# Optimization experiments

Measured on AMD Instinct MI355X. Metric: run time of the kernel, lower is better.

The kernel has to match this reference:

```python
import jax, jax.numpy as jnp
import numpy as np
from jax.ops import segment_sum, segment_min, segment_max

N, E = 25000, 400000
NF, EF = 30, 10
H = 40          # n_hidden (multiple of towers)
T = 5           # towers
F = H           # F_in per tower (divide_input=False)
FO = H // T     # F_out per tower
L = 2           # gnn layers
NC = 2          # classes
EPS_BN = 1e-5


def setup_inputs() -> dict:
    key = jax.random.key(0)
    ks = jax.random.split(key, 24)
    r = lambda k, s, sc=0.1: jax.random.normal(k, s, jnp.float32) * sc
    return {
        "x": jax.random.normal(ks[0], (N, NF), jnp.float32),
        "edge_attr": jax.random.normal(ks[1], (E, EF), jnp.float32),
        "edge_index": jax.random.randint(ks[2], (2, E), 0, N, jnp.int32),
        "node_w": r(ks[3], (NF, H)), "node_b": r(ks[4], (H,)),
        "edge_w": r(ks[5], (EF, H)), "edge_b": r(ks[6], (H,)),
        "enc_w": r(ks[7], (L, H, F)), "enc_b": r(ks[8], (L, F)),
        "pre_w": r(ks[9], (L, T, 3 * F, F)), "pre_b": r(ks[10], (L, T, F)),
        "post_w": r(ks[11], (L, T, 13 * F, FO)), "post_b": r(ks[12], (L, T, FO)),
        "lin_w": r(ks[13], (L, H, H)), "lin_b": r(ks[14], (L, H)),
        "bn_g": jnp.ones((L, H), jnp.float32), "bn_b": jnp.zeros((L, H), jnp.float32),
        "mlp1_w": r(ks[15], (3 * H, 50)), "mlp1_b": r(ks[16], (50,)),
        "mlp2_w": r(ks[17], (50, 25)), "mlp2_b": r(ks[18], (25,)),
        "mlp3_w": r(ks[19], (25, NC)), "mlp3_b": r(ks[20], (NC,)),
    }


def _pna_conv(x, src, dst, e_emb, enc_w, enc_b, pre_w, pre_b, post_w, post_b,
              lin_w, lin_b, cnt, cnt1, amp, att):
    # message: per-tower pre-MLP on cat(x_i=dst, x_j=src, enc(edge_attr))
    e = e_emb @ enc_w + enc_b                                    # [E, F]
    h = jnp.concatenate([x[dst], x[src], e], axis=-1)            # [E, 3F]
    hs = jnp.einsum('ef,tfo->eto', h, pre_w) + pre_b             # [E, T, F]
    # multi-aggregation over incoming edges (index = dst)
    c = cnt1[:, None, None]
    mean = segment_sum(hs, dst, num_segments=N) / c
    msq = segment_sum(hs * hs, dst, num_segments=N) / c
    std = jnp.sqrt(jax.nn.relu(msq - mean * mean) + 1e-5)
    has = (cnt > 0)[:, None, None]
    mn = jnp.where(has, segment_min(hs, dst, num_segments=N), 0.0)
    mx = jnp.where(has, segment_max(hs, dst, num_segments=N), 0.0)
    agg = jnp.concatenate([mean, mn, mx, std], axis=-1)          # [N, T, 4F]
    agg = jnp.concatenate([agg, agg * amp, agg * att], axis=-1)  # [N, T, 12F]
    out = jnp.concatenate(
        [jnp.broadcast_to(x[:, None, :], (N, T, F)), agg], axis=-1)  # [N, T, 13F]
    out = jnp.einsum('ntf,tfo->nto', out, post_w) + post_b       # [N, T, FO]
    return out.reshape(N, T * FO) @ lin_w + lin_b                # [N, H]


def reference(x, edge_attr, node_w, node_b, edge_w, edge_b, enc_w, enc_b,
              pre_w, pre_b, post_w, post_b, lin_w, lin_b, bn_g, bn_b,
              mlp1_w, mlp1_b, mlp2_w, mlp2_b, mlp3_w, mlp3_b, edge_index):
    src, dst = edge_index[0], edge_index[1]
    cnt = segment_sum(jnp.ones((E,), jnp.float32), dst, num_segments=N)  # in-degree
    cnt1 = jnp.maximum(cnt, 1.0)                                 # deg.clamp_(1)
    log_deg = jnp.log(cnt1 + 1.0)
    avg_log = jnp.mean(jnp.log(cnt + 1.0))                       # PNA avg_deg['log']
    amp = (log_deg / avg_log)[:, None, None]
    att = (avg_log / log_deg)[:, None, None]
    h = x @ node_w + node_b                                      # node embedding
    e_emb = edge_attr @ edge_w + edge_b                          # edge embedding
    for i in range(L):
        c = _pna_conv(h, src, dst, e_emb, enc_w[i], enc_b[i], pre_w[i], pre_b[i],
                      post_w[i], post_b[i], lin_w[i], lin_b[i], cnt, cnt1, amp, att)
        mu = jnp.mean(c, axis=0)
        var = jnp.mean((c - mu) ** 2, axis=0)                    # BatchNorm (batch stats)
        cbn = (c - mu) / jnp.sqrt(var + EPS_BN) * bn_g[i] + bn_b[i]
        h = (h + jax.nn.relu(cbn)) / 2.0
    z = jax.nn.relu(jnp.concatenate([h[src], h[dst]], axis=-1))  # [E, 2H]
    z = jnp.concatenate([z, e_emb], axis=-1)                     # [E, 3H]
    z = jax.nn.relu(z @ mlp1_w + mlp1_b)
    z = jax.nn.relu(z @ mlp2_w + mlp2_b)
    return z @ mlp3_w + mlp3_b                                   # [E, NC]
```

## Files before the change

kernel.cpp:

```cpp
#include <hip/hip_runtime.h>
#include <hip/hip_bf16.h>
#include <cstdint>
#include <cstddef>

#define NN 25000
#define NE 400000
#define NFD 30
#define EFD 10
#define H 40
#define T 5
#define FO 8
#define LAYERS 2
#define TF 200
#define PSTR 52
#define REC 12
#define WCN 416
#define WCK 64
#define SHP 72
#define NBLK (NN / 4)
#define SUPB ((NBLK + 63) / 64)
#define EPSV 1e-5f

typedef __attribute__((ext_vector_type(8))) short bf16x8;
typedef __attribute__((ext_vector_type(4))) float f32x4;

__device__ inline short bfbits(float v) {
    __hip_bfloat16 b = __float2bfloat16(v);
    return *(short*)&b;
}

__global__ __launch_bounds__(256) void k_front(const float* __restrict__ enc_w, const float* __restrict__ enc_b,
                                               const float* __restrict__ edge_w, const float* __restrict__ edge_b,
                                               const float* __restrict__ pre_w, const float* __restrict__ pre_b,
                                               const float* __restrict__ post_w,
                                               const float* __restrict__ w1, const float* __restrict__ b1,
                                               float* __restrict__ W3e, float* __restrict__ dvecF,
                                               __hip_bfloat16* __restrict__ Wcat,
                                               __hip_bfloat16* __restrict__ Wp4b, float* __restrict__ Wxd,
                                               float* __restrict__ W1e, float* __restrict__ b1e,
                                               const int* __restrict__ dst, int* __restrict__ cnt,
                                               const float* __restrict__ x, const float* __restrict__ node_w,
                                               const float* __restrict__ node_b, float* __restrict__ h,
                                               int grid1, int gdeg) {
    int blk = blockIdx.x;
    int tid = threadIdx.x;
    if (blk < 2 * grid1) {
        int layer = (blk >= grid1) ? 1 : 0;
        int id = (blk - layer * grid1) * 256 + tid;
        W3e   += (size_t)layer * EFD * TF;
        dvecF += (size_t)layer * TF;
        Wcat  += (size_t)layer * WCN * WCK;
        Wp4b  += (size_t)layer * 40 * 512;
        Wxd   += (size_t)layer * H * H;
        const int B0 = EFD * TF;
        const int B1 = B0 + WCN * WCK;
        const int B2 = B1 + EFD * 50;
        const int B3 = B2 + 40 * 512;
        const int B4 = B3 + H * H;
        if (id < B0) {
            int m = id / TF, j = id - m * TF;
            int t = j / H, f = j - t * H;
            const float* ew = enc_w + (size_t)layer * H * H;
            const float* pw = pre_w + (size_t)(layer * T + t) * 120 * H;
            float acc = 0.0f;
            for (int k = 0; k < H; k++) {
                float wk = edge_w[m * H + k];
                float g = 0.0f;
                #pragma unroll
                for (int o = 0; o < H; o++) g += ew[k * H + o] * pw[(80 + o) * H + f];
                acc += wk * g;
            }
            W3e[m * TF + j] = acc;
            if (m == 0) {
                const float* eb = enc_b + (size_t)layer * H;
                float dacc = pre_b[(size_t)(layer * T + t) * H + f];
                for (int o = 0; o < H; o++) {
                    float ebe = eb[o];
                    #pragma unroll
                    for (int k = 0; k < H; k++) ebe += edge_b[k] * ew[k * H + o];
                    dacc += ebe * pw[(80 + o) * H + f];
                }
                dvecF[j] = dacc;
            }
        } else if (id < B1) {
            int id2 = id - B0;
            int j = id2 / WCK, k = id2 - j * WCK;
            float val = 0.0f;
            if (k < H) {
                if (j < TF) {
                    int t = j / H, f = j - t * H;
                    val = pre_w[((size_t)(layer * T + t) * 120 + k) * H + f];
                } else if (j >= 208 && j < 208 + TF) {
                    int j2 = j - 208;
                    int t = j2 / H, f = j2 - t * H;
                    val = pre_w[((size_t)(layer * T + t) * 120 + H + k) * H + f];
                }
            }
            Wcat[id2] = __float2bfloat16(val);
        } else if (id < B2) {
            if (layer == 0) {
                int id2 = id - B1;
                int m = id2 / 50, o = id2 - m * 50;
                float acc = 0.0f;
                #pragma unroll
                for (int k = 0; k < H; k++) acc += edge_w[m * H + k] * w1[(80 + k) * 50 + o];
                W1e[m * 50 + o] = acc;
                if (m == 0) {
                    float bacc = b1[o];
                    #pragma unroll
                    for (int k = 0; k < H; k++) bacc += edge_b[k] * w1[(80 + k) * 50 + o];
                    b1e[o] = bacc;
                }
            }
        } else if (id < B3) {
            int i2 = id - B2;
            int fs4 = i2 >> 9;
            int rem = i2 & 511;
            int col = rem >> 2, c = rem & 3;
            int fs = fs4 * 4 + c;
            float v = 0.0f;
            if (col < 120) {
                int t = col / 24, r2 = col - t * 24;
                int grp = r2 >> 3, o = r2 & 7;
                v = post_w[((size_t)(layer * T + t) * 520 + 40 + grp * 160 + fs) * FO + o];
            }
            Wp4b[i2] = __float2bfloat16(v);
        } else if (id < B4) {
            int i2 = id - B3;
            int j = i2 / H, f = i2 - j * H;
            int t = j >> 3, o = j & 7;
            Wxd[i2] = post_w[((size_t)(layer * T + t) * 520 + f) * FO + o];
        }
    } else if (blk < 2 * grid1 + gdeg) {
        int e = (blk - 2 * grid1) * 256 + tid;
        if (e < NE) atomicAdd(&cnt[dst[e]], 1);
    } else {
        int id = (blk - 2 * grid1 - gdeg) * 256 + tid;
        if (id >= NN * H) return;
        int n = id / H, j = id - n * H;
        const float* xr = x + (size_t)n * NFD;
        float acc = node_b[j];
        #pragma unroll
        for (int m = 0; m < NFD; m++) acc += xr[m] * node_w[m * H + j];
        h[id] = acc;
    }
}

__global__ __launch_bounds__(1024) void k_scan(const int* __restrict__ cnt, int* __restrict__ offs,
                                               float* __restrict__ amp, float* __restrict__ att) {
    __shared__ int wsum[16];
    __shared__ float fsum[16];
    __shared__ float favg;
    int tid = threadIdx.x;
    int lane = tid & 63, wv = tid >> 6;
    {
        float s = 0.0f;
        for (int i = tid; i < NN; i += 1024) s += logf((float)cnt[i] + 1.0f);
        #pragma unroll
        for (int o = 32; o > 0; o >>= 1) s += __shfl_down(s, o);
        if (lane == 0) fsum[wv] = s;
        __syncthreads();
        if (tid == 0) {
            float a = 0.0f;
            #pragma unroll
            for (int i = 0; i < 16; i++) a += fsum[i];
            favg = a / (float)NN;
        }
        __syncthreads();
    }
    float avg = favg;
    int runbase = 0;
    for (int base = 0; base < NN; base += 4096) {
        int i0 = base + tid * 4;
        int4 v = make_int4(0, 0, 0, 0);
        if (i0 < NN) v = *(const int4*)(cnt + i0);
        if (i0 < NN) {
            #pragma unroll
            for (int c = 0; c < 4; c++) {
                int cv = (&v.x)[c];
                float c1 = fmaxf((float)cv, 1.0f);
                float lg = logf(c1 + 1.0f);
                amp[i0 + c] = lg / avg;
                att[i0 + c] = avg / lg;
            }
        }
        int tsum = v.x + v.y + v.z + v.w;
        int x = tsum;
        #pragma unroll
        for (int o = 1; o < 64; o <<= 1) {
            int y = __shfl_up(x, o);
            if (lane >= o) x += y;
        }
        if (lane == 63) wsum[wv] = x;
        __syncthreads();
        if (wv == 0 && lane < 16) {
            int wsv = wsum[lane];
            #pragma unroll
            for (int o = 1; o < 16; o <<= 1) {
                int y = __shfl_up(wsv, o);
                if (lane >= o) wsv += y;
            }
            wsum[lane] = wsv;
        }
        __syncthreads();
        int wpref = (wv > 0) ? wsum[wv - 1] : 0;
        int excl = runbase + wpref + x - tsum;
        if (i0 < NN) {
            offs[i0]     = excl;
            offs[i0 + 1] = excl + v.x;
            offs[i0 + 2] = excl + v.x + v.y;
            offs[i0 + 3] = excl + v.x + v.y + v.z;
        }
        runbase += wsum[15];
        __syncthreads();
    }
    if (tid == 0) offs[NN] = runbase;
}

__global__ __launch_bounds__(256) void k_mid(const int* __restrict__ src, const int* __restrict__ dst,
                                             const float* __restrict__ edge_attr,
                                             const int* __restrict__ offs, int* __restrict__ fill,
                                             float* __restrict__ ea_csr, int* __restrict__ pdst,
                                             const float* __restrict__ h,
                                             const __hip_bfloat16* __restrict__ Wcat,
                                             float* __restrict__ A, __hip_bfloat16* __restrict__ Bbf,
                                             int gab) {
    __shared__ short sh[64 * SHP];
    int blk = blockIdx.x;
    int tid = threadIdx.x;
    if (blk < gab) {
        int n0 = blk * 64;
        int nodes = NN - n0; if (nodes > 64) nodes = 64;
        for (int i = tid; i < 64 * SHP; i += 256) sh[i] = 0;
        __syncthreads();
        for (int i = tid; i < nodes * H; i += 256) {
            int f = i % H;
            sh[(i / H) * SHP + f] = bfbits(h[(size_t)n0 * H + i]);
        }
        __syncthreads();

        int wv = tid >> 6, lane = tid & 63;
        int q = lane >> 4, c16 = lane & 15;
        const short* arow = sh + (wv * 16 + c16) * SHP + q * 8;
        bf16x8 a0 = *(const bf16x8*)(arow);
        bf16x8 a1 = *(const bf16x8*)(arow + 32);
        int gm = n0 + wv * 16 + q * 4;

        for (int jt = 0; jt < 26; jt++) {
            int col = jt * 16 + c16;
            const short* wrow = (const short*)Wcat + (size_t)col * WCK + q * 8;
            bf16x8 b0 = *(const bf16x8*)(wrow);
            bf16x8 b1 = *(const bf16x8*)(wrow + 32);
            f32x4 acc = {0.0f, 0.0f, 0.0f, 0.0f};
            acc = __builtin_amdgcn_mfma_f32_16x16x32_bf16(a0, b0, acc, 0, 0, 0);
            acc = __builtin_amdgcn_mfma_f32_16x16x32_bf16(a1, b1, acc, 0, 0, 0);
            if (col < TF) {
                #pragma unroll
                for (int r = 0; r < 4; r++) {
                    int row = gm + r;
                    if (row < NN) A[(size_t)row * TF + col] = acc[r];
                }
            } else if (col >= 208) {
                int c2 = col - 208;
                if (c2 < TF) {
                    #pragma unroll
                    for (int r = 0; r < 4; r++) {
                        int row = gm + r;
                        if (row < NN) Bbf[(size_t)row * TF + c2] = __float2bfloat16(acc[r]);
                    }
                }
            }
        }
    } else {
        int e = (blk - gab) * 256 + tid;
        if (e >= NE) return;
        int d = dst[e];
        int p = offs[d] + atomicAdd(&fill[d], 1);
        const float2* ear = (const float2*)(edge_attr + (size_t)e * EFD);
        float2 v0 = ear[0], v1 = ear[1], v2 = ear[2], v3 = ear[3], v4 = ear[4];
        float4* o = (float4*)(ea_csr + (size_t)p * REC);
        o[0] = make_float4(v0.x, v0.y, v1.x, v1.y);
        o[1] = make_float4(v2.x, v2.y, v3.x, v3.y);
        o[2] = make_float4(v4.x, v4.y, __int_as_float(src[e]), __int_as_float(e));
        pdst[p] = d;
    }
}

__global__ __launch_bounds__(256) void k_abm(float* h, const float* __restrict__ cbuf,
                                             const float* __restrict__ partials2,
                                             const float* __restrict__ bng, const float* __restrict__ bnb,
                                             const __hip_bfloat16* __restrict__ Wcat,
                                             float* __restrict__ A, __hip_bfloat16* __restrict__ Bbf) {
    __shared__ short sh[64 * SHP];
    __shared__ float bns[80];
    int tid = threadIdx.x;
    int n0 = blockIdx.x * 64;
    int nodes = NN - n0; if (nodes > 64) nodes = 64;
    if (tid < 80) {
        float s = 0.0f;
        for (int i = 0; i < SUPB; i++) s += partials2[i * 80 + tid];
        bns[tid] = s;
    }
    for (int i = tid; i < 64 * SHP; i += 256) sh[i] = 0;
    __syncthreads();
    float invN = 1.0f / (float)NN;
    for (int i = tid; i < nodes * H; i += 256) {
        int f = i % H;
        float hv = h[(size_t)n0 * H + i];
        float mu = bns[f] * invN;
        float var = bns[40 + f] * invN - mu * mu;
        float c = (cbuf[(size_t)n0 * H + i] - mu) * rsqrtf(var + EPSV) * bng[f] + bnb[f];
        float hn = (hv + fmaxf(c, 0.0f)) * 0.5f;
        h[(size_t)n0 * H + i] = hn;
        sh[(i / H) * SHP + f] = bfbits(hn);
    }
    __syncthreads();

    int wv = tid >> 6, lane = tid & 63;
    int q = lane >> 4, c16 = lane & 15;
    const short* arow = sh + (wv * 16 + c16) * SHP + q * 8;
    bf16x8 a0 = *(const bf16x8*)(arow);
    bf16x8 a1 = *(const bf16x8*)(arow + 32);
    int gm = n0 + wv * 16 + q * 4;

    for (int jt = 0; jt < 26; jt++) {
        int col = jt * 16 + c16;
        const short* wrow = (const short*)Wcat + (size_t)col * WCK + q * 8;
        bf16x8 b0 = *(const bf16x8*)(wrow);
        bf16x8 b1 = *(const bf16x8*)(wrow + 32);
        f32x4 acc = {0.0f, 0.0f, 0.0f, 0.0f};
        acc = __builtin_amdgcn_mfma_f32_16x16x32_bf16(a0, b0, acc, 0, 0, 0);
        acc = __builtin_amdgcn_mfma_f32_16x16x32_bf16(a1, b1, acc, 0, 0, 0);
        if (col < TF) {
            #pragma unroll
            for (int r = 0; r < 4; r++) {
                int row = gm + r;
                if (row < NN) A[(size_t)row * TF + col] = acc[r];
            }
        } else if (col >= 208) {
            int c2 = col - 208;
            if (c2 < TF) {
                #pragma unroll
                for (int r = 0; r < 4; r++) {
                    int row = gm + r;
                    if (row < NN) Bbf[(size_t)row * TF + c2] = __float2bfloat16(acc[r]);
                }
            }
        }
    }
}

__global__ __launch_bounds__(256) void k_agg(const float* __restrict__ ea_csr,
                                             const __hip_bfloat16* __restrict__ Bbf,
                                             const float* __restrict__ A, const float* __restrict__ w3e,
                                             const float* __restrict__ dvecF, const int* __restrict__ cnt,
                                             const int* __restrict__ offs,
                                             const float* __restrict__ h,
                                             const __hip_bfloat16* __restrict__ Wp4b, const float* __restrict__ Wxd,
                                             const float* __restrict__ pbL,
                                             const float* __restrict__ amp, const float* __restrict__ att,
                                             const float* __restrict__ lwL, const float* __restrict__ lbL,
                                             float* __restrict__ cbuf, float* __restrict__ partials2) {
    __shared__ float sst[4 * 800];
    __shared__ float shh[4 * H];
    float* spart = sst;
    float* scp   = sst + 1024;
    float* lred  = sst + 1280;
    int tid = threadIdx.x;
    int lane = tid & 63;
    int wv = tid >> 6;
    int n0 = blockIdx.x * 4;
    int n = __builtin_amdgcn_readfirstlane(n0 + wv);
    if (tid < 4 * H) shh[tid] = h[(size_t)n0 * H + tid];
    int deg = cnt[n];
    int start = offs[n];
    bool comp = lane < TF / 4;
    float4 w3q[EFD];
    float4 dj4 = make_float4(0, 0, 0, 0), a4 = make_float4(0, 0, 0, 0);
    if (comp) {
        #pragma unroll
        for (int m = 0; m < EFD; m++) w3q[m] = *(const float4*)(w3e + m * TF + 4 * lane);
        dj4 = *(const float4*)(dvecF + 4 * lane);
        a4  = *(const float4*)(A + (size_t)n * TF + 4 * lane);
    }
    float sx = 0, sy = 0, sz = 0, sw_ = 0;
    float qx = 0, qy = 0, qz = 0, qw = 0;
    float mnx = 3.4e38f, mny = 3.4e38f, mnz = 3.4e38f, mnw = 3.4e38f;
    float mxx = -3.4e38f, mxy = -3.4e38f, mxz = -3.4e38f, mxw = -3.4e38f;
    const float4* recb = (const float4*)ea_csr + (size_t)start * 3;
    const uint16_t* Bu = (const uint16_t*)Bbf;

    auto edge = [&](float4 qa, float4 qb, float4 qc, uint2 bv) {
        float b0 = __uint_as_float(bv.x << 16);
        float b1 = __uint_as_float(bv.x & 0xffff0000u);
        float b2 = __uint_as_float(bv.y << 16);
        float b3 = __uint_as_float(bv.y & 0xffff0000u);
        float eav[EFD] = {qa.x, qa.y, qa.z, qa.w, qb.x, qb.y, qb.z, qb.w, qc.x, qc.y};
        float cx = dj4.x, cy = dj4.y, cz = dj4.z, cw = dj4.w;
        #pragma unroll
        for (int m = 0; m < EFD; m++) {
            cx = fmaf(eav[m], w3q[m].x, cx);
            cy = fmaf(eav[m], w3q[m].y, cy);
            cz = fmaf(eav[m], w3q[m].z, cz);
            cw = fmaf(eav[m], w3q[m].w, cw);
        }
        float ux = b0 + cx, uy = b1 + cy, uz = b2 + cz, uw = b3 + cw;
        sx += ux; qx = fmaf(ux, ux, qx); mnx = fminf(mnx, ux); mxx = fmaxf(mxx, ux);
        sy += uy; qy = fmaf(uy, uy, qy); mny = fminf(mny, uy); mxy = fmaxf(mxy, uy);
        sz += uz; qz = fmaf(uz, uz, qz); mnz = fminf(mnz, uz); mxz = fmaxf(mxz, uz);
        sw_ += uw; qw = fmaf(uw, uw, qw); mnw = fminf(mnw, uw); mxw = fmaxf(mxw, uw);
    };

    int r = 0;
    for (; r + 4 <= deg; r += 4) {
        float4 qa0 = recb[(r + 0) * 3], qb0 = recb[(r + 0) * 3 + 1], qc0 = recb[(r + 0) * 3 + 2];
        float4 qa1 = recb[(r + 1) * 3], qb1 = recb[(r + 1) * 3 + 1], qc1 = recb[(r + 1) * 3 + 2];
        float4 qa2 = recb[(r + 2) * 3], qb2 = recb[(r + 2) * 3 + 1], qc2 = recb[(r + 2) * 3 + 2];
        float4 qa3 = recb[(r + 3) * 3], qb3 = recb[(r + 3) * 3 + 1], qc3 = recb[(r + 3) * 3 + 2];
        int s0 = __float_as_int(qc0.z), s1 = __float_as_int(qc1.z);
        int s2 = __float_as_int(qc2.z), s3 = __float_as_int(qc3.z);
        if (comp) {
            uint2 v0 = *(const uint2*)(Bu + (size_t)s0 * TF + 4 * lane);
            uint2 v1 = *(const uint2*)(Bu + (size_t)s1 * TF + 4 * lane);
            uint2 v2 = *(const uint2*)(Bu + (size_t)s2 * TF + 4 * lane);
            uint2 v3 = *(const uint2*)(Bu + (size_t)s3 * TF + 4 * lane);
            edge(qa0, qb0, qc0, v0);
            edge(qa1, qb1, qc1, v1);
            edge(qa2, qb2, qc2, v2);
            edge(qa3, qb3, qc3, v3);
        }
    }
    for (; r < deg; r++) {
        float4 qa = recb[r * 3], qb = recb[r * 3 + 1], qc = recb[r * 3 + 2];
        int sn = __float_as_int(qc.z);
        if (comp) {
            uint2 bv = *(const uint2*)(Bu + (size_t)sn * TF + 4 * lane);
            edge(qa, qb, qc, bv);
        }
    }
    if (comp) {
        float d = (float)deg, c1 = fmaxf(d, 1.0f);
        float inv = 1.0f / c1;
        float mex = (d * a4.x + sx) * inv, mey = (d * a4.y + sy) * inv;
        float mez = (d * a4.z + sz) * inv, mew = (d * a4.w + sw_) * inv;
        float msx = (d * a4.x * a4.x + 2.0f * a4.x * sx + qx) * inv;
        float msy = (d * a4.y * a4.y + 2.0f * a4.y * sy + qy) * inv;
        float msz = (d * a4.z * a4.z + 2.0f * a4.z * sz + qz) * inv;
        float msw = (d * a4.w * a4.w + 2.0f * a4.w * sw_ + qw) * inv;
        float4 mean4 = make_float4(mex, mey, mez, mew);
        float4 sd4 = make_float4(sqrtf(fmaxf(msx - mex * mex, 0.0f) + EPSV),
                                 sqrtf(fmaxf(msy - mey * mey, 0.0f) + EPSV),
                                 sqrtf(fmaxf(msz - mez * mez, 0.0f) + EPSV),
                                 sqrtf(fmaxf(msw - mew * mew, 0.0f) + EPSV));
        bool has = deg > 0;
        float4 mnv4 = has ? make_float4(a4.x + mnx, a4.y + mny, a4.z + mnz, a4.w + mnw)
                          : make_float4(0, 0, 0, 0);
        float4 mxv4 = has ? make_float4(a4.x + mxx, a4.y + mxy, a4.z + mxz, a4.w + mxw)
                          : make_float4(0, 0, 0, 0);
        int j0 = 4 * lane;
        int t = j0 / H, f = j0 - t * H;
        float* sb = sst + wv * 800 + t * 160 + f;
        *(float4*)(sb)       = mean4;
        *(float4*)(sb + 40)  = mnv4;
        *(float4*)(sb + 80)  = mxv4;
        *(float4*)(sb + 120) = sd4;
    }
    __syncthreads();

    {
        int op = tid & 127, half = tid >> 7;
        int tt = op / 24; if (tt > 4) tt = 4;
        const uint16_t* wtp = (const uint16_t*)Wp4b + (size_t)(half * 20) * 512 + op * 4;
        const float* sb0 = sst + tt * 160 + half * 80;
        float p0 = 0, p1 = 0, p2 = 0, p3 = 0;
        #pragma unroll 4
        for (int k = 0; k < 20; k++) {
            uint2 wb = *(const uint2*)(wtp + (size_t)k * 512);
            float wx = __uint_as_float(wb.x << 16);
            float wy = __uint_as_float(wb.x & 0xffff0000u);
            float wz = __uint_as_float(wb.y << 16);
            float ww = __uint_as_float(wb.y & 0xffff0000u);
            const float* sp = sb0 + k * 4;
            float4 v0 = *(const float4*)(sp);
            float4 v1 = *(const float4*)(sp + 800);
            float4 v2 = *(const float4*)(sp + 1600);
            float4 v3 = *(const float4*)(sp + 2400);
            p0 += v0.x * wx + v0.y * wy + v0.z * wz + v0.w * ww;
            p1 += v1.x * wx + v1.y * wy + v1.z * wz + v1.w * ww;
            p2 += v2.x * wx + v2.y * wy + v2.z * wz + v2.w * ww;
            p3 += v3.x * wx + v3.y * wy + v3.z * wz + v3.w * ww;
        }
        __syncthreads();
        if (op < 120) {
            spart[(0 * 120 + op) * 2 + half] = p0;
            spart[(1 * 120 + op) * 2 + half] = p1;
            spart[(2 * 120 + op) * 2 + half] = p2;
            spart[(3 * 120 + op) * 2 + half] = p3;
        }
    }
    __syncthreads();

    if (tid < 160) {
        int nd = tid / H, j = tid - nd * H;
        int t = j >> 3, o = j & 7;
        int ng = n0 + nd;
        float am = amp[ng], at = att[ng];
        const float* yr = spart + (nd * 120 + t * 24) * 2;
        float pa = yr[o * 2]        + yr[o * 2 + 1];
        float pb = yr[(8 + o) * 2]  + yr[(8 + o) * 2 + 1];
        float pc = yr[(16 + o) * 2] + yr[(16 + o) * 2 + 1];
        float acc = pbL[j] + pa + am * pb + at * pc;
        const float* hr = shh + nd * H;
        const float* wx = Wxd + (size_t)j * H;
        #pragma unroll
        for (int fq = 0; fq < 10; fq++) {
            float4 hv = *(const float4*)(hr + fq * 4);
            float4 wv = *(const float4*)(wx + fq * 4);
            acc += hv.x * wv.x + hv.y * wv.y + hv.z * wv.z + hv.w * wv.w;
        }
        scp[tid] = acc;
    }
    __syncthreads();

    if (tid < 160) {
        int nd = tid / H, j = tid - nd * H;
        const float* scr = scp + nd * H;
        float lacc = lbL[j];
        #pragma unroll
        for (int k = 0; k < H; k++) lacc = fmaf(scr[k], lwL[k * H + j], lacc);
        cbuf[(size_t)(n0 + nd) * H + j] = lacc;
        lred[tid] = lacc;
    }
    __syncthreads();

    if (tid < 80) {
        int c2 = tid / 40, j = tid - c2 * 40;
        float s = 0.0f;
        #pragma unroll
        for (int nd = 0; nd < 4; nd++) {
            float v = lred[nd * 40 + j];
            s += c2 ? v * v : v;
        }
        atomicAdd(&partials2[(size_t)(blockIdx.x >> 6) * 80 + tid], s);
    }
}

__global__ __launch_bounds__(256) void k_prep2(const float* __restrict__ h, const float* __restrict__ cbuf,
                                               const float* __restrict__ partials2,
                                               const float* __restrict__ bng, const float* __restrict__ bnb,
                                               const float* __restrict__ w1,
                                               float* __restrict__ P1, float* __restrict__ P2) {
    __shared__ float bns[80];
    __shared__ float sh[50 * H];
    int tid = threadIdx.x;
    int n0 = blockIdx.x * 50;
    if (tid < 80) {
        float s = 0.0f;
        for (int i = 0; i < SUPB; i++) s += partials2[i * 80 + tid];
        bns[tid] = s;
    }
    __syncthreads();
    float invN = 1.0f / (float)NN;
    for (int idx = tid; idx < 50 * H; idx += 256) {
        int j = idx % H;
        float mu = bns[j] * invN;
        float var = bns[40 + j] * invN - mu * mu;
        float inv = rsqrtf(var + EPSV);
        float cv = (cbuf[(size_t)n0 * H + idx] - mu) * inv * bng[j] + bnb[j];
        sh[idx] = (h[(size_t)n0 * H + idx] + fmaxf(cv, 0.0f)) * 0.5f;
    }
    __syncthreads();
    for (int idx = tid; idx < 50 * 50; idx += 256) {
        int nl = idx / 50, o = idx - nl * 50;
        const float* hr = sh + nl * H;
        float a1 = 0.0f, a2 = 0.0f;
        #pragma unroll
        for (int f = 0; f < H; f++) {
            float v = fmaxf(hr[f], 0.0f);
            a1 += v * w1[f * 50 + o];
            a2 += v * w1[(H + f) * 50 + o];
        }
        P1[(size_t)(n0 + nl) * PSTR + o] = a1;
        P2[(size_t)(n0 + nl) * PSTR + o] = a2;
    }
}

__global__ __launch_bounds__(256) void k_mlp(const float* __restrict__ ea_csr, const int* __restrict__ pdst,
                                             const float* __restrict__ P1, const float* __restrict__ P2,
                                             const float* __restrict__ W1e, const float* __restrict__ b1e,
                                             const float* __restrict__ w2, const float* __restrict__ b2,
                                             const float* __restrict__ w3, const float* __restrict__ b3,
                                             float* __restrict__ out) {
    int p = blockIdx.x * 256 + threadIdx.x;
    if (p >= NE) return;
    const float4* rec = (const float4*)ea_csr + (size_t)p * 3;
    float4 r0 = rec[0], r1 = rec[1], r2 = rec[2];
    int s = __float_as_int(r2.z), eid = __float_as_int(r2.w);
    int d = pdst[p];
    float ea[EFD] = {r0.x, r0.y, r0.z, r0.w, r1.x, r1.y, r1.z, r1.w, r2.x, r2.y};

    float z1[52];
    const float4* p1r = (const float4*)(P1 + (size_t)s * PSTR);
    const float4* p2r = (const float4*)(P2 + (size_t)d * PSTR);
    #pragma unroll
    for (int i = 0; i < 13; i++) {
        float4 a = p1r[i], b = p2r[i];
        z1[4 * i]     = a.x + b.x;
        z1[4 * i + 1] = a.y + b.y;
        z1[4 * i + 2] = a.z + b.z;
        z1[4 * i + 3] = a.w + b.w;
    }
    #pragma unroll
    for (int k = 0; k < 50; k++) z1[k] += b1e[k];
    #pragma unroll
    for (int m = 0; m < EFD; m++) {
        float v = ea[m];
        #pragma unroll
        for (int k = 0; k < 50; k++) z1[k] = fmaf(v, W1e[m * 50 + k], z1[k]);
    }
    float z2[25];
    #pragma unroll
    for (int o = 0; o < 25; o++) z2[o] = b2[o];
    #pragma unroll
    for (int k = 0; k < 50; k++) {
        float v = fmaxf(z1[k], 0.0f);
        #pragma unroll
        for (int o = 0; o < 25; o++) z2[o] = fmaf(v, w2[k * 25 + o], z2[o]);
    }
    float o0 = b3[0], o1 = b3[1];
    #pragma unroll
    for (int k = 0; k < 25; k++) {
        float v = fmaxf(z2[k], 0.0f);
        o0 = fmaf(v, w3[k * 2], o0);
        o1 = fmaf(v, w3[k * 2 + 1], o1);
    }
    *(float2*)(out + (size_t)eid * 2) = make_float2(o0, o1);
}

extern "C" void kernel_launch(void* const* d_in, const int* in_sizes, int n_in,
                              void* d_out, int out_size, void* d_ws, size_t ws_size,
                              hipStream_t stream) {
    const float* x         = (const float*)d_in[0];
    const float* edge_attr = (const float*)d_in[1];
    const int*   eidx      = (const int*)  d_in[2];
    const float* node_w    = (const float*)d_in[3];
    const float* node_b    = (const float*)d_in[4];
    const float* edge_w    = (const float*)d_in[5];
    const float* edge_b    = (const float*)d_in[6];
    const float* enc_w     = (const float*)d_in[7];
    const float* enc_b     = (const float*)d_in[8];
    const float* pre_w     = (const float*)d_in[9];
    const float* pre_b     = (const float*)d_in[10];
    const float* post_w    = (const float*)d_in[11];
    const float* post_b    = (const float*)d_in[12];
    const float* lin_w     = (const float*)d_in[13];
    const float* lin_b     = (const float*)d_in[14];
    const float* bn_g      = (const float*)d_in[15];
    const float* bn_b      = (const float*)d_in[16];
    const float* w1 = (const float*)d_in[17];
    const float* b1 = (const float*)d_in[18];
    const float* w2 = (const float*)d_in[19];
    const float* b2 = (const float*)d_in[20];
    const float* w3 = (const float*)d_in[21];
    const float* b3 = (const float*)d_in[22];
    const int* srcp = eidx;
    const int* dstp = eidx + NE;
    float* out = (float*)d_out;

    char* ws = (char*)d_ws;
    size_t off = 0;
    auto alloc = [&](size_t bytes) -> char* {
        char* p = ws + off;
        off += (bytes + 255) & ~(size_t)255;
        return p;
    };
    float* h      = (float*)alloc((size_t)NN * H * 4);
    float* Abuf   = (float*)alloc((size_t)NN * TF * 4);
    float* cbuf   = (float*)alloc((size_t)NN * H * 4);
    __hip_bfloat16* Bbf = (__hip_bfloat16*)alloc((size_t)NN * TF * 2 + 256);
    float* ea_csr = (float*)alloc((size_t)NE * REC * 4);
    int* pdst     = (int*)alloc((size_t)NE * 4);
    float* W3e    = (float*)alloc((size_t)LAYERS * EFD * TF * 4);
    float* dvecF  = (float*)alloc((size_t)LAYERS * TF * 4);
    __hip_bfloat16* Wcat = (__hip_bfloat16*)alloc((size_t)LAYERS * WCN * WCK * 2);
    __hip_bfloat16* Wp4b = (__hip_bfloat16*)alloc((size_t)LAYERS * 40 * 512 * 2);
    float* Wxd    = (float*)alloc((size_t)LAYERS * H * H * 4);
    float* P1     = (float*)alloc((size_t)NN * PSTR * 4);
    float* P2     = (float*)alloc((size_t)NN * PSTR * 4);
    float* W1e    = (float*)alloc((size_t)EFD * 50 * 4);
    float* b1e    = (float*)alloc((size_t)64 * 4);
    float* amp    = (float*)alloc((size_t)NN * 4);
    float* att    = (float*)alloc((size_t)NN * 4);
    int* offs     = (int*)alloc((size_t)(NN + 1) * 4);
    size_t zoff = off;
    int* cnt_i    = (int*)alloc((size_t)NN * 4);
    int* fill     = (int*)alloc((size_t)NN * 4);
    float* partials2 = (float*)alloc((size_t)LAYERS * SUPB * 80 * 4);
    size_t zsize = off - zoff;
    if (off > ws_size) return;

    hipMemsetAsync(cnt_i, 0, zsize, stream);

    int prep1_tot = EFD * TF + WCN * WCK + EFD * 50 + 40 * 512 + H * H;
    int prep1_grid = (prep1_tot + 255) / 256;
    int gdeg = (NE + 255) / 256;
    int gh0 = (NN * H + 255) / 256;
    k_front<<<2 * prep1_grid + gdeg + gh0, 256, 0, stream>>>(
        enc_w, enc_b, edge_w, edge_b, pre_w, pre_b, post_w, w1, b1,
        W3e, dvecF, Wcat, Wp4b, Wxd, W1e, b1e,
        dstp, cnt_i, x, node_w, node_b, h, prep1_grid, gdeg);

    k_scan<<<1, 1024, 0, stream>>>(cnt_i, offs, amp, att);

    int gab = (NN + 63) / 64;
    int gsc = (NE + 255) / 256;
    k_mid<<<gab + gsc, 256, 0, stream>>>(srcp, dstp, edge_attr, offs, fill, ea_csr, pdst,
                                         h, Wcat, Abuf, Bbf, gab);

    for (int layer = 0; layer < LAYERS; layer++) {
        if (layer > 0) {
            k_abm<<<gab, 256, 0, stream>>>(
                h, cbuf, partials2, bn_g, bn_b,
                Wcat + (size_t)WCN * WCK, Abuf, Bbf);
        }
        k_agg<<<NBLK, 256, 0, stream>>>(ea_csr, Bbf, Abuf,
                                        W3e + (size_t)layer * EFD * TF,
                                        dvecF + (size_t)layer * TF,
                                        cnt_i, offs, h,
                                        Wp4b + (size_t)layer * 40 * 512,
                                        Wxd + (size_t)layer * H * H,
                                        post_b + (size_t)layer * T * FO,
                                        amp, att,
                                        lin_w + (size_t)layer * H * H, lin_b + (size_t)layer * H,
                                        cbuf, partials2 + (size_t)layer * SUPB * 80);
    }
    k_prep2<<<NN / 50, 256, 0, stream>>>(h, cbuf, partials2 + (size_t)SUPB * 80,
                                         bn_g + H, bn_b + H, w1, P1, P2);
    k_mlp<<<(NE + 255) / 256, 256, 0, stream>>>(ea_csr, pdst, P1, P2, W1e, b1e, w2, b2, w3, b3, out);
}
```

Baseline: 482.3 us.

## Split each node's edge aggregation across two wavefronts and merge via LDS

k_agg now launches 512 threads per block so that two wavefronts share each destination node. They process interleaved groups of four edges, and one wavefront merges the other's sum, sum-of-squares, min and max partials through a new shared buffer before computing the statistics. This halves the serial per-node edge loop and exposes more memory-level parallelism for the gathers. The cost is extra LDS, an added barrier, and half the threads sitting idle in the later dense stages. Per-edge VGPR-heavy work at 512 threads may also limit occupancy.

New measurement: 737.0 us. +52.8%, slower.

```diff
diff --git a/kernel.cpp b/kernel.cpp
--- a/kernel.cpp
+++ b/kernel.cpp
@@ -350,7 +350,7 @@
     }
 }
 
-__global__ __launch_bounds__(256) void k_agg(const float* __restrict__ ea_csr,
+__global__ __launch_bounds__(512) void k_agg(const float* __restrict__ ea_csr,
                                              const __hip_bfloat16* __restrict__ Bbf,
                                              const float* __restrict__ A, const float* __restrict__ w3e,
                                              const float* __restrict__ dvecF, const int* __restrict__ cnt,
@@ -363,14 +363,17 @@
                                              float* __restrict__ cbuf, float* __restrict__ partials2) {
     __shared__ float sst[4 * 800];
     __shared__ float shh[4 * H];
+    __shared__ float mrg[4 * 16 * 52];
     float* spart = sst;
     float* scp   = sst + 1024;
     float* lred  = sst + 1280;
     int tid = threadIdx.x;
     int lane = tid & 63;
     int wv = tid >> 6;
+    int nd = wv >> 1;
+    int sub = wv & 1;
     int n0 = blockIdx.x * 4;
-    int n = __builtin_amdgcn_readfirstlane(n0 + wv);
+    int n = __builtin_amdgcn_readfirstlane(n0 + nd);
     if (tid < 4 * H) shh[tid] = h[(size_t)n0 * H + tid];
     int deg = cnt[n];
     int start = offs[n];
@@ -411,8 +414,8 @@
         sw_ += uw; qw = fmaf(uw, uw, qw); mnw = fminf(mnw, uw); mxw = fmaxf(mxw, uw);
     };
 
-    int r = 0;
-    for (; r + 4 <= deg; r += 4) {
+    int r = sub * 4;
+    for (; r + 4 <= deg; r += 8) {
         float4 qa0 = recb[(r + 0) * 3], qb0 = recb[(r + 0) * 3 + 1], qc0 = recb[(r + 0) * 3 + 2];
         float4 qa1 = recb[(r + 1) * 3], qb1 = recb[(r + 1) * 3 + 1], qc1 = recb[(r + 1) * 3 + 2];
         float4 qa2 = recb[(r + 2) * 3], qb2 = recb[(r + 2) * 3 + 1], qc2 = recb[(r + 2) * 3 + 2];
@@ -430,15 +433,33 @@
             edge(qa3, qb3, qc3, v3);
         }
     }
-    for (; r < deg; r++) {
-        float4 qa = recb[r * 3], qb = recb[r * 3 + 1], qc = recb[r * 3 + 2];
-        int sn = __float_as_int(qc.z);
-        if (comp) {
-            uint2 bv = *(const uint2*)(Bu + (size_t)sn * TF + 4 * lane);
-            edge(qa, qb, qc, bv);
-        }
-    }
-    if (comp) {
+    if (sub == 0) {
+        for (int rr = deg & ~3; rr < deg; rr++) {
+            float4 qa = recb[rr * 3], qb = recb[rr * 3 + 1], qc = recb[rr * 3 + 2];
+            int sn = __float_as_int(qc.z);
+            if (comp) {
+                uint2 bv = *(const uint2*)(Bu + (size_t)sn * TF + 4 * lane);
+                edge(qa, qb, qc, bv);
+            }
+        }
+    }
+    if (comp && sub == 1) {
+        float* mb = mrg + (nd * 16) * 52 + lane;
+        mb[0 * 52] = sx;  mb[1 * 52] = sy;  mb[2 * 52] = sz;  mb[3 * 52] = sw_;
+        mb[4 * 52] = qx;  mb[5 * 52] = qy;  mb[6 * 52] = qz;  mb[7 * 52] = qw;
+        mb[8 * 52] = mnx; mb[9 * 52] = mny; mb[10 * 52] = mnz; mb[11 * 52] = mnw;
+        mb[12 * 52] = mxx; mb[13 * 52] = mxy; mb[14 * 52] = mxz; mb[15 * 52] = mxw;
+    }
+    __syncthreads();
+    if (comp && sub == 0) {
+        const float* mb = mrg + (nd * 16) * 52 + lane;
+        sx += mb[0 * 52];  sy += mb[1 * 52];  sz += mb[2 * 52];  sw_ += mb[3 * 52];
+        qx += mb[4 * 52];  qy += mb[5 * 52];  qz += mb[6 * 52];  qw += mb[7 * 52];
+        mnx = fminf(mnx, mb[8 * 52]);  mny = fminf(mny, mb[9 * 52]);
+        mnz = fminf(mnz, mb[10 * 52]); mnw = fminf(mnw, mb[11 * 52]);
+        mxx = fmaxf(mxx, mb[12 * 52]); mxy = fmaxf(mxy, mb[13 * 52]);
+        mxz = fmaxf(mxz, mb[14 * 52]); mxw = fmaxf(mxw, mb[15 * 52]);
+
         float d = (float)deg, c1 = fmaxf(d, 1.0f);
         float inv = 1.0f / c1;
         float mex = (d * a4.x + sx) * inv, mey = (d * a4.y + sy) * inv;
@@ -459,7 +480,7 @@
                           : make_float4(0, 0, 0, 0);
         int j0 = 4 * lane;
         int t = j0 / H, f = j0 - t * H;
-        float* sb = sst + wv * 800 + t * 160 + f;
+        float* sb = sst + nd * 800 + t * 160 + f;
         *(float4*)(sb)       = mean4;
         *(float4*)(sb + 40)  = mnv4;
         *(float4*)(sb + 80)  = mxv4;
@@ -467,12 +488,12 @@
     }
     __syncthreads();
 
-    {
-        int op = tid & 127, half = tid >> 7;
+    float p0 = 0, p1 = 0, p2 = 0, p3 = 0;
+    int op = tid & 127, half = (tid >> 7) & 1;
+    if (tid < 256) {
         int tt = op / 24; if (tt > 4) tt = 4;
         const uint16_t* wtp = (const uint16_t*)Wp4b + (size_t)(half * 20) * 512 + op * 4;
         const float* sb0 = sst + tt * 160 + half * 80;
-        float p0 = 0, p1 = 0, p2 = 0, p3 = 0;
         #pragma unroll 4
         for (int k = 0; k < 20; k++) {
             uint2 wb = *(const uint2*)(wtp + (size_t)k * 512);
@@ -490,27 +511,27 @@
             p2 += v2.x * wx + v2.y * wy + v2.z * wz + v2.w * ww;
             p3 += v3.x * wx + v3.y * wy + v3.z * wz + v3.w * ww;
         }
-        __syncthreads();
-        if (op < 120) {
-            spart[(0 * 120 + op) * 2 + half] = p0;
-            spart[(1 * 120 + op) * 2 + half] = p1;
-            spart[(2 * 120 + op) * 2 + half] = p2;
-            spart[(3 * 120 + op) * 2 + half] = p3;
-        }
+    }
+    __syncthreads();
+    if (tid < 256 && op < 120) {
+        spart[(0 * 120 + op) * 2 + half] = p0;
+        spart[(1 * 120 + op) * 2 + half] = p1;
+        spart[(2 * 120 + op) * 2 + half] = p2;
+        spart[(3 * 120 + op) * 2 + half] = p3;
     }
     __syncthreads();
 
     if (tid < 160) {
-        int nd = tid / H, j = tid - nd * H;
+        int ndc = tid / H, j = tid - ndc * H;
         int t = j >> 3, o = j & 7;
-        int ng = n0 + nd;
+        int ng = n0 + ndc;
         float am = amp[ng], at = att[ng];
-        const float* yr = spart + (nd * 120 + t * 24) * 2;
+        const float* yr = spart + (ndc * 120 + t * 24) * 2;
         float pa = yr[o * 2]        + yr[o * 2 + 1];
         float pb = yr[(8 + o) * 2]  + yr[(8 + o) * 2 + 1];
         float pc = yr[(16 + o) * 2] + yr[(16 + o) * 2 + 1];
         float acc = pbL[j] + pa + am * pb + at * pc;
-        const float* hr = shh + nd * H;
+        const float* hr = shh + ndc * H;
         const float* wx = Wxd + (size_t)j * H;
         #pragma unroll
         for (int fq = 0; fq < 10; fq++) {
@@ -523,12 +544,12 @@
     __syncthreads();
 
     if (tid < 160) {
-        int nd = tid / H, j = tid - nd * H;
-        const float* scr = scp + nd * H;
+        int ndc = tid / H, j = tid - ndc * H;
+        const float* scr = scp + ndc * H;
         float lacc = lbL[j];
         #pragma unroll
         for (int k = 0; k < H; k++) lacc = fmaf(scr[k], lwL[k * H + j], lacc);
-        cbuf[(size_t)(n0 + nd) * H + j] = lacc;
+        cbuf[(size_t)(n0 + ndc) * H + j] = lacc;
         lred[tid] = lacc;
     }
     __syncthreads();
@@ -537,8 +558,8 @@
         int c2 = tid / 40, j = tid - c2 * 40;
         float s = 0.0f;
         #pragma unroll
-        for (int nd = 0; nd < 4; nd++) {
-            float v = lred[nd * 40 + j];
+        for (int ndc = 0; ndc < 4; ndc++) {
+            float v = lred[ndc * 40 + j];
             s += c2 ? v * v : v;
         }
         atomicAdd(&partials2[(size_t)(blockIdx.x >> 6) * 80 + tid], s);
@@ -723,7 +744,7 @@
                 h, cbuf, partials2, bn_g, bn_b,
                 Wcat + (size_t)WCN * WCK, Abuf, Bbf);
         }
-        k_agg<<<NBLK, 256, 0, stream>>>(ea_csr, Bbf, Abuf,
+        k_agg<<<NBLK, 512, 0, stream>>>(ea_csr, Bbf, Abuf,
                                         W3e + (size_t)layer * EFD * TF,
                                         dvecF + (size_t)layer * TF,
                                         cnt_i, offs, h,
```
